# Optimization experiments

Hardware: AMD Instinct MI355X
Metric: run time of the kernel (lower is better)

## Reference

```python
import jax, jax.numpy as jnp
import numpy as np

EPS = 1e-12  # torch F.normalize default eps


def _l2norm(t, axis=-1):
    n = jnp.sqrt(jnp.sum(t * t, axis=axis, keepdims=True))
    return t / jnp.maximum(n, EPS)


def setup_inputs() -> dict:
    key = jax.random.key(0)
    ks = jax.random.split(key, 5)
    B, N, C, H = 8, 4096, 1024, 16
    x = jax.random.normal(ks[0], (B, N, C), dtype=jnp.float32)
    # nn.Linear(dim, 3*dim, bias=False): weight [3C, C]; we store transposed [C, 3C]
    w_qkv = jax.random.normal(ks[1], (C, 3 * C), dtype=jnp.float32) * (1.0 / np.sqrt(C))
    temperature = jnp.ones((H, 1, 1), dtype=jnp.float32)
    w_proj = jax.random.normal(ks[2], (C, C), dtype=jnp.float32) * (1.0 / np.sqrt(C))
    b_proj = jax.random.normal(ks[3], (C,), dtype=jnp.float32) * 0.01
    return {"x": x, "w_qkv": w_qkv, "temperature": temperature,
            "w_proj": w_proj, "b_proj": b_proj}


def reference(x, w_qkv, temperature, w_proj, b_proj):
    B, N, C = x.shape
    H = temperature.shape[0]
    dh = C // H
    # qkv: [B, N, 3C] -> [B, N, 3, H, dh] -> q/k/v each [B, H, dh, N]
    qkv = (x @ w_qkv).reshape(B, N, 3, H, dh).transpose(2, 0, 3, 4, 1)
    q, k, v = qkv[0], qkv[1], qkv[2]
    # L2-normalize over token axis (last dim)
    q = _l2norm(q)
    k = _l2norm(k)
    # channel-channel attention: [B, H, dh, dh]
    attn = jnp.einsum("bhdn,bhen->bhde", q, k) * temperature  # temp broadcasts [H,1,1]
    attn = jax.nn.softmax(attn, axis=-1)
    # weighted sum over channels: [B, H, dh, N] -> [B, N, C]
    out = jnp.einsum("bhde,bhen->bhdn", attn, v).transpose(0, 3, 1, 2).reshape(B, N, C)
    return out @ w_proj + b_proj
```

## Files before the change

### kernel.cpp

```cpp
#include <hip/hip_runtime.h>
#include <cstdint>

typedef unsigned short u16;
typedef unsigned int u32;
typedef __attribute__((ext_vector_type(8))) short bf16x8;
typedef __attribute__((ext_vector_type(4))) float f32x4;

typedef const u32 __attribute__((address_space(1)))* gp_t;
typedef u32 __attribute__((address_space(3)))* lp_t;

__device__ __forceinline__ u16 f2bf(float f) {
    union { float f; u32 u; } v; v.f = f;
    u32 r = v.u + 0x7FFFu + ((v.u >> 16) & 1u);
    return (u16)(r >> 16);
}
__device__ __forceinline__ float bf2f(u16 h) {
    union { u32 u; float f; } v; v.u = ((u32)h) << 16;
    return v.f;
}

__global__ void k_pack_x(const float* __restrict__ x, u16* __restrict__ xb, int n4) {
    int stride = gridDim.x * blockDim.x;
    for (int i = blockIdx.x * blockDim.x + threadIdx.x; i < n4; i += stride) {
        float4 v = ((const float4*)x)[i];
        ushort4 o;
        o.x = f2bf(v.x); o.y = f2bf(v.y); o.z = f2bf(v.z); o.w = f2bf(v.w);
        ((ushort4*)xb)[i] = o;
    }
}

__global__ void k_transpose_w(const float* __restrict__ src, u16* __restrict__ dst, int ncols) {
    __shared__ float t[64][65];
    int ntn = ncols >> 6;
    int kb = (blockIdx.x / ntn) * 64;
    int nb = (blockIdx.x % ntn) * 64;
    for (int i = threadIdx.x; i < 4096; i += 256) {
        int r = i >> 6, c = i & 63;
        t[r][c] = src[(long)(kb + r) * ncols + nb + c];
    }
    __syncthreads();
    for (int i = threadIdx.x; i < 4096; i += 256) {
        int r = i >> 6, c = i & 63;
        dst[(long)(nb + r) * 1024 + kb + c] = f2bf(t[c][r]);
    }
}

template<int EPI>
__global__ __launch_bounds__(512, 2) void k_gemm(
    const u16* __restrict__ A, const u16* __restrict__ Bt,
    int nTilesN,
    u16* __restrict__ qkT, u16* __restrict__ v_tm,
    float* __restrict__ outp, const float* __restrict__ bias)
{
    __shared__ uint4 smem4[8704];
    u16* sm = (u16*)smem4;

    const int tid = threadIdx.x;
    const int wid = tid >> 6, lane = tid & 63;
    const int wr = wid >> 2, wc = wid & 3;
    const int fr = lane & 15, sl = lane >> 4;

    const int nwg = gridDim.x;
    const int cpx = nwg >> 3;
    const int logical = (blockIdx.x & 7) * cpx + (blockIdx.x >> 3);

    long m0; int n0;
    const u16* BtEff = Bt;
    if (EPI == 0) {
        const int bn = logical % nTilesN;
        m0 = (long)(logical / nTilesN) * 256;
        n0 = bn * 256;
    } else {
        const int b = logical >> 6;
        const int mt = (logical >> 2) & 15;
        const int nt = logical & 3;
        m0 = (long)b * 4096 + mt * 256;
        n0 = nt * 256;
        BtEff = Bt + ((long)b << 20);
    }

    const int srow = wid * 32 + (lane >> 2);
    const int kswz = (((lane & 3) ^ ((srow >> 1) & 3)) << 3);
    const u16* gA = A + (m0 + srow) * 1024L + kswz;
    const u16* gB = BtEff + ((long)n0 + srow) * 1024L + kswz;
    const int ldst = wid * 1024;

    const int fxor = ((sl ^ ((fr >> 1) & 3)) << 3);
    const int aBase = (wr * 128 + fr) * 32 + fxor;
    const int bBase = 32768 + (wc * 64 + fr) * 32 + fxor;

    f32x4 acc[8][4];
#pragma unroll
    for (int i = 0; i < 8; ++i)
#pragma unroll
        for (int j = 0; j < 4; ++j) acc[i][j] = (f32x4){0.f, 0.f, 0.f, 0.f};

#define STAGE_A(d, kh, ts) do { \
    const u16* g_ = gA + (ts) * 64 + (kh) * 32; \
    u16* l_ = sm + (d) * 16384 + (kh) * 8192 + ldst; \
    __builtin_amdgcn_global_load_lds((gp_t)g_, (lp_t)l_, 16, 0, 0); \
    __builtin_amdgcn_global_load_lds((gp_t)(g_ + 16 * 1024), (lp_t)(l_ + 512), 16, 0, 0); \
} while (0)
#define STAGE_B(d, kh, ts) do { \
    const u16* g_ = gB + (ts) * 64 + (kh) * 32; \
    u16* l_ = sm + 32768 + (d) * 16384 + (kh) * 8192 + ldst; \
    __builtin_amdgcn_global_load_lds((gp_t)g_, (lp_t)l_, 16, 0, 0); \
    __builtin_amdgcn_global_load_lds((gp_t)(g_ + 16 * 1024), (lp_t)(l_ + 512), 16, 0, 0); \
} while (0)

    STAGE_A(0, 0, 0); STAGE_B(0, 0, 0);
    STAGE_A(0, 1, 0); STAGE_B(0, 1, 0);
    STAGE_A(1, 0, 1); STAGE_B(1, 0, 1);
    asm volatile("s_waitcnt vmcnt(8)" ::: "memory");
    __builtin_amdgcn_s_barrier();

    bf16x8 afX[4], afY[4], bfX[4], bfY[4];
#pragma unroll
    for (int ni = 0; ni < 4; ++ni) bfX[ni] = *(const bf16x8*)(sm + bBase + ni * 512);
#pragma unroll
    for (int mi = 0; mi < 4; ++mi) afX[mi] = *(const bf16x8*)(sm + aBase + mi * 512);

#pragma unroll 2
    for (int T = 0; T < 16; ++T) {
        const int d = T & 1;
        const int t1 = (T + 1 < 16) ? T + 1 : 15;
        const int t2 = (T + 2 < 16) ? T + 2 : 15;
        const int base = d * 16384;
        const int nbase = (d ^ 1) * 16384;

#pragma unroll
        for (int mi = 0; mi < 4; ++mi)
            afY[mi] = *(const bf16x8*)(sm + aBase + (4 + mi) * 512 + base);
        STAGE_A(d ^ 1, 1, t1);
        asm volatile("s_waitcnt vmcnt(6)" ::: "memory");
        __builtin_amdgcn_s_barrier();
        __builtin_amdgcn_s_setprio(1);
#pragma unroll
        for (int mi = 0; mi < 4; ++mi)
#pragma unroll
            for (int ni = 0; ni < 4; ++ni)
                acc[mi][ni] = __builtin_amdgcn_mfma_f32_16x16x32_bf16(afX[mi], bfX[ni], acc[mi][ni], 0, 0, 0);
        __builtin_amdgcn_s_setprio(0);
        __builtin_amdgcn_s_barrier();

#pragma unroll
        for (int ni = 0; ni < 4; ++ni)
            bfY[ni] = *(const bf16x8*)(sm + bBase + ni * 512 + base + 8192);
#pragma unroll
        for (int mi = 0; mi < 4; ++mi)
            afX[mi] = *(const bf16x8*)(sm + aBase + mi * 512 + base + 8192);
        STAGE_B(d ^ 1, 1, t1);
        __builtin_amdgcn_s_barrier();
        __builtin_amdgcn_s_setprio(1);
#pragma unroll
        for (int mi = 0; mi < 4; ++mi)
#pragma unroll
            for (int ni = 0; ni < 4; ++ni)
                acc[mi + 4][ni] = __builtin_amdgcn_mfma_f32_16x16x32_bf16(afY[mi], bfX[ni], acc[mi + 4][ni], 0, 0, 0);
        __builtin_amdgcn_s_setprio(0);
        __builtin_amdgcn_s_barrier();

#pragma unroll
        for (int mi = 0; mi < 4; ++mi)
            afY[mi] = *(const bf16x8*)(sm + aBase + (4 + mi) * 512 + base + 8192);
        STAGE_A(d, 0, t2);
        asm volatile("s_waitcnt vmcnt(6)" ::: "memory");
        __builtin_amdgcn_s_barrier();
        __builtin_amdgcn_s_setprio(1);
#pragma unroll
        for (int mi = 0; mi < 4; ++mi)
#pragma unroll
            for (int ni = 0; ni < 4; ++ni)
                acc[mi][ni] = __builtin_amdgcn_mfma_f32_16x16x32_bf16(afX[mi], bfY[ni], acc[mi][ni], 0, 0, 0);
        __builtin_amdgcn_s_setprio(0);
        __builtin_amdgcn_s_barrier();

#pragma unroll
        for (int ni = 0; ni < 4; ++ni)
            bfX[ni] = *(const bf16x8*)(sm + bBase + ni * 512 + nbase);
#pragma unroll
        for (int mi = 0; mi < 4; ++mi)
            afX[mi] = *(const bf16x8*)(sm + aBase + mi * 512 + nbase);
        STAGE_B(d, 0, t2);
        __builtin_amdgcn_s_barrier();
        __builtin_amdgcn_s_setprio(1);
#pragma unroll
        for (int mi = 0; mi < 4; ++mi)
#pragma unroll
            for (int ni = 0; ni < 4; ++ni)
                acc[mi + 4][ni] = __builtin_amdgcn_mfma_f32_16x16x32_bf16(afY[mi], bfY[ni], acc[mi + 4][ni], 0, 0, 0);
        __builtin_amdgcn_s_setprio(0);
        __builtin_amdgcn_s_barrier();
    }
#undef STAGE_A
#undef STAGE_B
    asm volatile("s_waitcnt vmcnt(0)" ::: "memory");
    __syncthreads();

    if (EPI == 0) {
        const long b = m0 >> 12;
        const int tok0 = (int)(m0 & 4095);
        if (n0 < 2048) {
            u16* piece = sm + wid * 8704;
#pragma unroll
            for (int mi = 0; mi < 8; ++mi)
#pragma unroll
                for (int ni = 0; ni < 4; ++ni) {
                    const int ch = ni * 16 + fr;
                    const int tk = mi * 16 + sl * 4;
                    ushort4 w;
                    w.x = f2bf(acc[mi][ni][0]); w.y = f2bf(acc[mi][ni][1]);
                    w.z = f2bf(acc[mi][ni][2]); w.w = f2bf(acc[mi][ni][3]);
                    *(ushort4*)(piece + ch * 136 + tk) = w;
                }
            __syncthreads();
#pragma unroll
            for (int i = 0; i < 16; ++i) {
                const int chunk = i * 512 + tid;
                const int row = chunk >> 4, c16 = chunk & 15;
                const int p = row >> 6, chl = row & 63;
                const int wrp = p >> 2, wcp = p & 3;
                const uint4 v = *(const uint4*)(sm + p * 8704 + chl * 136 + c16 * 8);
                *(uint4*)(qkT + ((b * 2048 + n0 + wcp * 64 + chl) * 4096L + tok0 + wrp * 128 + c16 * 8)) = v;
            }
        } else {
            u16* piece = sm + wid * 8704;
#pragma unroll
            for (int mi = 0; mi < 8; ++mi)
#pragma unroll
                for (int ni = 0; ni < 4; ++ni) {
                    const int ch = ni * 16 + fr;
                    const int tk = mi * 16 + sl * 4;
#pragma unroll
                    for (int r = 0; r < 4; ++r)
                        piece[(tk + r) * 68 + ch] = f2bf(acc[mi][ni][r]);
                }
            __syncthreads();
#pragma unroll
            for (int i = 0; i < 32; ++i) {
                const int chunk = i * 512 + tid;
                const int row = chunk >> 4, c8 = chunk & 15;
                const int p = row >> 7, tk = row & 127;
                const int wrp = p >> 2, wcp = p & 3;
                const uint2 v = *(const uint2*)(sm + p * 8704 + tk * 68 + c8 * 4);
                *(uint2*)(v_tm + ((b * 4096 + tok0 + wrp * 128 + tk) * 1024L + (n0 - 2048) + wcp * 64 + c8 * 4)) = v;
            }
        }
    } else {
        float bi[4];
#pragma unroll
        for (int ni = 0; ni < 4; ++ni) bi[ni] = bias[n0 + wc * 64 + ni * 16 + fr];
#pragma unroll
        for (int pass = 0; pass < 2; ++pass) {
            float* pieceF = (float*)smem4 + wid * 4352;
            if (pass) __syncthreads();
#pragma unroll
            for (int mi2 = 0; mi2 < 4; ++mi2) {
                const int mi = pass * 4 + mi2;
#pragma unroll
                for (int ni = 0; ni < 4; ++ni) {
                    const int ch = ni * 16 + fr;
                    const int tk = mi2 * 16 + sl * 4;
#pragma unroll
                    for (int r = 0; r < 4; ++r)
                        pieceF[(tk + r) * 68 + ch] = acc[mi][ni][r] + bi[ni];
                }
            }
            __syncthreads();
#pragma unroll
            for (int i = 0; i < 16; ++i) {
                const int chunk = i * 512 + tid;
                const int row = chunk >> 4, c4 = chunk & 15;
                const int p = row >> 6, tk = row & 63;
                const int wrp = p >> 2, wcp = p & 3;
                const float4 v = *(const float4*)((float*)smem4 + p * 4352 + tk * 68 + c4 * 4);
                *(float4*)(outp + (m0 + wrp * 128 + pass * 64 + tk) * 1024L + n0 + wcp * 64 + c4 * 4) = v;
            }
        }
    }
}

__global__ __launch_bounds__(512, 2) void k_gram(
    const u16* __restrict__ qkT, float* __restrict__ gram_part, float* __restrict__ sq_part)
{
    __shared__ u16 lQ[64 * 256];
    __shared__ u16 lK[64 * 256];

    const int blk = blockIdx.x;
    const int seg = blk & 15;
    const int bh = blk >> 4;
    const int b = bh >> 4, h = bh & 15;
    const int tid = threadIdx.x;
    const int wid = tid >> 6, lane = tid & 63;

    {
        const int r2 = lane >> 5;
        const int slot = lane & 31;
        const int rbase = wid * 8;
#pragma unroll
        for (int i = 0; i < 4; ++i) {
            const int r = rbase + i * 2 + r2;
            const int col = seg * 256 + ((slot ^ (r & 7)) << 3);
            const u16* gq = qkT + ((long)(b * 2048 + h * 64 + r)) * 4096 + col;
            const u16* gk = qkT + ((long)(b * 2048 + 1024 + h * 64 + r)) * 4096 + col;
            __builtin_amdgcn_global_load_lds((gp_t)gq, (lp_t)(lQ + (rbase + i * 2) * 256), 16, 0, 0);
            __builtin_amdgcn_global_load_lds((gp_t)gk, (lp_t)(lK + (rbase + i * 2) * 256), 16, 0, 0);
        }
    }
    __syncthreads();

    {
        const int row = tid >> 2, q4 = tid & 3;
        const u16* src = (row < 64 ? lQ + row * 256 : lK + (row - 64) * 256) + q4 * 64;
        float s = 0.f;
#pragma unroll
        for (int i = 0; i < 8; ++i) {
            uint4 v = *(const uint4*)(src + i * 8);
            float a0, a1;
            a0 = bf2f((u16)(v.x & 0xFFFF)); a1 = bf2f((u16)(v.x >> 16)); s += a0 * a0 + a1 * a1;
            a0 = bf2f((u16)(v.y & 0xFFFF)); a1 = bf2f((u16)(v.y >> 16)); s += a0 * a0 + a1 * a1;
            a0 = bf2f((u16)(v.z & 0xFFFF)); a1 = bf2f((u16)(v.z >> 16)); s += a0 * a0 + a1 * a1;
            a0 = bf2f((u16)(v.w & 0xFFFF)); a1 = bf2f((u16)(v.w >> 16)); s += a0 * a0 + a1 * a1;
        }
        s += __shfl_xor(s, 1);
        s += __shfl_xor(s, 2);
        if (q4 == 0) sq_part[(long)blk * 128 + row] = s;
    }

    const int mrow = wid >> 1, npair = wid & 1;
    const int fr = lane & 15, sl = lane >> 4;
    f32x4 acc[2];
    acc[0] = (f32x4){0.f, 0.f, 0.f, 0.f};
    acc[1] = (f32x4){0.f, 0.f, 0.f, 0.f};
#pragma unroll
    for (int ks = 0; ks < 8; ++ks) {
        const int ra = mrow * 16 + fr;
        const bf16x8 a = *(const bf16x8*)(lQ + ra * 256 + (((ks * 4 + sl) ^ (ra & 7)) << 3));
#pragma unroll
        for (int ni = 0; ni < 2; ++ni) {
            const int rb = npair * 32 + ni * 16 + fr;
            const bf16x8 bb = *(const bf16x8*)(lK + rb * 256 + (((ks * 4 + sl) ^ (rb & 7)) << 3));
            acc[ni] = __builtin_amdgcn_mfma_f32_16x16x32_bf16(a, bb, acc[ni], 0, 0, 0);
        }
    }
    float* gp = gram_part + (long)blk * 4096;
#pragma unroll
    for (int ni = 0; ni < 2; ++ni)
#pragma unroll
        for (int r = 0; r < 4; ++r)
            gp[(mrow * 16 + sl * 4 + r) * 64 + npair * 32 + ni * 16 + fr] = acc[ni][r];
}

__global__ __launch_bounds__(256) void k_smax(
    const float* __restrict__ gram_part, const float* __restrict__ sq_part,
    const float* __restrict__ temperature, u16* __restrict__ attn_g)
{
    const int row = blockIdx.x * 4 + (threadIdx.x >> 6);
    const int e = threadIdx.x & 63;
    const int bh = row >> 6, d = row & 63;
    const int h = bh & 15;
    float raw = 0.f, sqq = 0.f, sqk = 0.f;
    const float* gp = gram_part + (long)bh * 16 * 4096 + d * 64 + e;
    const float* sp = sq_part + (long)bh * 16 * 128;
#pragma unroll
    for (int s = 0; s < 16; ++s) {
        raw += gp[s * 4096];
        sqq += sp[s * 128 + d];
        sqk += sp[s * 128 + 64 + e];
    }
    const float rq = 1.f / fmaxf(sqrtf(sqq), 1e-12f);
    const float rk = 1.f / fmaxf(sqrtf(sqk), 1e-12f);
    const float v = raw * rq * rk * temperature[h];
    float mx = v;
#pragma unroll
    for (int o = 32; o; o >>= 1) mx = fmaxf(mx, __shfl_xor(mx, o));
    const float p = __expf(v - mx);
    float sum = p;
#pragma unroll
    for (int o = 32; o; o >>= 1) sum += __shfl_xor(sum, o);
    attn_g[(long)row * 64 + e] = f2bf(p / sum);
}

__global__ __launch_bounds__(256) void k_wmix(
    const u16* __restrict__ attn_g, const u16* __restrict__ wpT, u16* __restrict__ wmix)
{
    __shared__ u16 lA[64 * 72];
    __shared__ u16 lB[256 * 64];

    const int blk = blockIdx.x;
    const int nseg = blk & 3, bh = blk >> 2;
    const int b = bh >> 4, h = bh & 15;
    const int tid = threadIdx.x;
    const int wid = tid >> 6, lane = tid & 63;
    const int fr = lane & 15, sl = lane >> 4;

#pragma unroll
    for (int i = 0; i < 8; ++i) {
        const int cc = wid * 8 + i;
        const int row = cc * 8 + (lane >> 3);
        const int slot = lane & 7;
        const u16* g = wpT + (long)(nseg * 256 + row) * 1024 + h * 64 + ((slot ^ (row & 7)) << 3);
        __builtin_amdgcn_global_load_lds((gp_t)g, (lp_t)(lB + cc * 512), 16, 0, 0);
    }
    {
        const u16* src = attn_g + (long)bh * 4096;
        for (int i = tid; i < 4096; i += 256) {
            const int d = i >> 6, e = i & 63;
            lA[e * 72 + d] = src[i];
        }
    }
    __syncthreads();

    f32x4 acc[4][4];
#pragma unroll
    for (int i = 0; i < 4; ++i)
#pragma unroll
        for (int j = 0; j < 4; ++j) acc[i][j] = (f32x4){0.f, 0.f, 0.f, 0.f};

#pragma unroll
    for (int ks = 0; ks < 2; ++ks) {
        bf16x8 a[4], bb[4];
#pragma unroll
        for (int mi = 0; mi < 4; ++mi)
            a[mi] = *(const bf16x8*)(lA + (mi * 16 + fr) * 72 + ks * 32 + sl * 8);
#pragma unroll
        for (int ni = 0; ni < 4; ++ni) {
            const int rb = wid * 64 + ni * 16 + fr;
            bb[ni] = *(const bf16x8*)(lB + rb * 64 + (((ks * 4 + sl) ^ (rb & 7)) << 3));
        }
#pragma unroll
        for (int mi = 0; mi < 4; ++mi)
#pragma unroll
            for (int ni = 0; ni < 4; ++ni)
                acc[mi][ni] = __builtin_amdgcn_mfma_f32_16x16x32_bf16(a[mi], bb[ni], acc[mi][ni], 0, 0, 0);
    }

    u16* dst = wmix + ((long)b << 20);
#pragma unroll
    for (int mi = 0; mi < 4; ++mi)
#pragma unroll
        for (int ni = 0; ni < 4; ++ni) {
            const int cout = nseg * 256 + wid * 64 + ni * 16 + fr;
            const int e0 = mi * 16 + sl * 4;
            ushort4 w;
            w.x = f2bf(acc[mi][ni][0]); w.y = f2bf(acc[mi][ni][1]);
            w.z = f2bf(acc[mi][ni][2]); w.w = f2bf(acc[mi][ni][3]);
            *(ushort4*)(dst + (long)cout * 1024 + h * 64 + e0) = w;
        }
}

extern "C" void kernel_launch(void* const* d_in, const int* in_sizes, int n_in,
                              void* d_out, int out_size, void* d_ws, size_t ws_size,
                              hipStream_t stream) {
    const float* x = (const float*)d_in[0];
    const float* w_qkv = (const float*)d_in[1];
    const float* temperature = (const float*)d_in[2];
    const float* w_proj = (const float*)d_in[3];
    const float* b_proj = (const float*)d_in[4];
    float* out = (float*)d_out;
    char* ws = (char*)d_ws;

    u16* wqT   = (u16*)(ws);
    u16* wpT   = (u16*)(ws + 6291456);
    u16* xb    = (u16*)(ws + 8388608);
    u16* qkT   = (u16*)(ws + 75497472);
    u16* v_tm  = (u16*)(ws + 209715200);
    u16* attn_g = (u16*)(ws + 276889600);
    float* gram_part = (float*)(ws + 8388608);
    float* sq_part   = (float*)(ws + 41943040);
    u16* wmix = (u16*)(ws + 8388608);

    k_pack_x<<<2048, 256, 0, stream>>>(x, xb, 8388608);
    k_transpose_w<<<768, 256, 0, stream>>>(w_qkv, wqT, 3072);
    k_transpose_w<<<256, 256, 0, stream>>>(w_proj, wpT, 1024);
    k_gemm<0><<<1536, 512, 0, stream>>>(xb, wqT, 12, qkT, v_tm, nullptr, nullptr);
    k_gram<<<2048, 512, 0, stream>>>(qkT, gram_part, sq_part);
    k_smax<<<2048, 256, 0, stream>>>(gram_part, sq_part, temperature, attn_g);
    k_wmix<<<512, 256, 0, stream>>>(attn_g, wpT, wmix);
    k_gemm<1><<<512, 512, 0, stream>>>(v_tm, wmix, 4, nullptr, nullptr, out, b_proj);
}
```

Before: 392.1 us.

## Fold V projection into per-batch output weights, skip materializing V

Instead of computing V = x·Wv for every token and then multiplying by the per-batch mixed weights, the V weight slice is packed separately and multiplied with the per-batch attention-mixed projection weights (a small 1024x1024 GEMM per batch). The final GEMM then reads x directly with the fused per-batch weight. This removes a third of the large QKV GEMM and the V write/readback, at the cost of an extra small batched GEMM and re-reading x in the final GEMM.

```diff
diff --git a/kernel.cpp b/kernel.cpp
--- a/kernel.cpp
+++ b/kernel.cpp
@@ -43,6 +43,17 @@
         int r = i >> 6, c = i & 63;
         dst[(long)(nb + r) * 1024 + kb + c] = f2bf(t[c][r]);
     }
+}
+
+__global__ __launch_bounds__(256) void k_pack_wv(const float* __restrict__ wqkv, u16* __restrict__ wvb) {
+    const int idx = blockIdx.x * 256 + threadIdx.x;
+    const int cin = idx >> 7, e0 = (idx & 127) * 8;
+    const float4 v1 = *(const float4*)(wqkv + (long)cin * 3072 + 2048 + e0);
+    const float4 v2 = *(const float4*)(wqkv + (long)cin * 3072 + 2048 + e0 + 4);
+    u16 u[8];
+    u[0] = f2bf(v1.x); u[1] = f2bf(v1.y); u[2] = f2bf(v1.z); u[3] = f2bf(v1.w);
+    u[4] = f2bf(v2.x); u[5] = f2bf(v2.y); u[6] = f2bf(v2.z); u[7] = f2bf(v2.w);
+    *(uint4*)(wvb + (long)cin * 1024 + e0) = *(const uint4*)u;
 }
 
 template<int EPI>
@@ -64,25 +75,14 @@
     const int cpx = nwg >> 3;
     const int logical = (blockIdx.x & 7) * cpx + (blockIdx.x >> 3);
 
-    long m0; int n0;
-    const u16* BtEff = Bt;
-    if (EPI == 0) {
-        const int bn = logical % nTilesN;
-        m0 = (long)(logical / nTilesN) * 256;
-        n0 = bn * 256;
-    } else {
-        const int b = logical >> 6;
-        const int mt = (logical >> 2) & 15;
-        const int nt = logical & 3;
-        m0 = (long)b * 4096 + mt * 256;
-        n0 = nt * 256;
-        BtEff = Bt + ((long)b << 20);
-    }
+    const int bn = logical % nTilesN;
+    const long m0 = (long)(logical / nTilesN) * 256;
+    const int n0 = bn * 256;
 
     const int srow = wid * 32 + (lane >> 2);
     const int kswz = (((lane & 3) ^ ((srow >> 1) & 3)) << 3);
     const u16* gA = A + (m0 + srow) * 1024L + kswz;
-    const u16* gB = BtEff + ((long)n0 + srow) * 1024L + kswz;
+    const u16* gB = Bt + ((long)n0 + srow) * 1024L + kswz;
     const int ldst = wid * 1024;
 
     const int fxor = ((sl ^ ((fr >> 1) & 3)) << 3);
@@ -200,82 +200,27 @@
     if (EPI == 0) {
         const long b = m0 >> 12;
         const int tok0 = (int)(m0 & 4095);
-        if (n0 < 2048) {
-            u16* piece = sm + wid * 8704;
-#pragma unroll
-            for (int mi = 0; mi < 8; ++mi)
-#pragma unroll
-                for (int ni = 0; ni < 4; ++ni) {
-                    const int ch = ni * 16 + fr;
-                    const int tk = mi * 16 + sl * 4;
-                    ushort4 w;
-                    w.x = f2bf(acc[mi][ni][0]); w.y = f2bf(acc[mi][ni][1]);
-                    w.z = f2bf(acc[mi][ni][2]); w.w = f2bf(acc[mi][ni][3]);
-                    *(ushort4*)(piece + ch * 136 + tk) = w;
-                }
-            __syncthreads();
-#pragma unroll
-            for (int i = 0; i < 16; ++i) {
-                const int chunk = i * 512 + tid;
-                const int row = chunk >> 4, c16 = chunk & 15;
-                const int p = row >> 6, chl = row & 63;
-                const int wrp = p >> 2, wcp = p & 3;
-                const uint4 v = *(const uint4*)(sm + p * 8704 + chl * 136 + c16 * 8);
-                *(uint4*)(qkT + ((b * 2048 + n0 + wcp * 64 + chl) * 4096L + tok0 + wrp * 128 + c16 * 8)) = v;
+        u16* piece = sm + wid * 8704;
+#pragma unroll
+        for (int mi = 0; mi < 8; ++mi)
+#pragma unroll
+            for (int ni = 0; ni < 4; ++ni) {
+                const int ch = ni * 16 + fr;
+                const int tk = mi * 16 + sl * 4;
+                ushort4 w;
+                w.x = f2bf(acc[mi][ni][0]); w.y = f2bf(acc[mi][ni][1]);
+                w.z = f2bf(acc[mi][ni][2]); w.w = f2bf(acc[mi][ni][3]);
+                *(ushort4*)(piece + ch * 136 + tk) = w;
             }
-        } else {
-            u16* piece = sm + wid * 8704;
-#pragma unroll
-            for (int mi = 0; mi < 8; ++mi)
-#pragma unroll
-                for (int ni = 0; ni < 4; ++ni) {
-                    const int ch = ni * 16 + fr;
-                    const int tk = mi * 16 + sl * 4;
-#pragma unroll
-                    for (int r = 0; r < 4; ++r)
-                        piece[(tk + r) * 68 + ch] = f2bf(acc[mi][ni][r]);
-                }
-            __syncthreads();
-#pragma unroll
-            for (int i = 0; i < 32; ++i) {
-                const int chunk = i * 512 + tid;
-                const int row = chunk >> 4, c8 = chunk & 15;
-                const int p = row >> 7, tk = row & 127;
-                const int wrp = p >> 2, wcp = p & 3;
-                const uint2 v = *(const uint2*)(sm + p * 8704 + tk * 68 + c8 * 4);
-                *(uint2*)(v_tm + ((b * 4096 + tok0 + wrp * 128 + tk) * 1024L + (n0 - 2048) + wcp * 64 + c8 * 4)) = v;
-            }
-        }
-    } else {
-        float bi[4];
-#pragma unroll
-        for (int ni = 0; ni < 4; ++ni) bi[ni] = bias[n0 + wc * 64 + ni * 16 + fr];
-#pragma unroll
-        for (int pass = 0; pass < 2; ++pass) {
-            float* pieceF = (float*)smem4 + wid * 4352;
-            if (pass) __syncthreads();
-#pragma unroll
-            for (int mi2 = 0; mi2 < 4; ++mi2) {
-                const int mi = pass * 4 + mi2;
-#pragma unroll
-                for (int ni = 0; ni < 4; ++ni) {
-                    const int ch = ni * 16 + fr;
-                    const int tk = mi2 * 16 + sl * 4;
-#pragma unroll
-                    for (int r = 0; r < 4; ++r)
-                        pieceF[(tk + r) * 68 + ch] = acc[mi][ni][r] + bi[ni];
-                }
-            }
-            __syncthreads();
-#pragma unroll
-            for (int i = 0; i < 16; ++i) {
-                const int chunk = i * 512 + tid;
-                const int row = chunk >> 4, c4 = chunk & 15;
-                const int p = row >> 6, tk = row & 63;
-                const int wrp = p >> 2, wcp = p & 3;
-                const float4 v = *(const float4*)((float*)smem4 + p * 4352 + tk * 68 + c4 * 4);
-                *(float4*)(outp + (m0 + wrp * 128 + pass * 64 + tk) * 1024L + n0 + wcp * 64 + c4 * 4) = v;
-            }
+        __syncthreads();
+#pragma unroll
+        for (int i = 0; i < 16; ++i) {
+            const int chunk = i * 512 + tid;
+            const int row = chunk >> 4, c16 = chunk & 15;
+            const int p = row >> 6, chl = row & 63;
+            const int wrp = p >> 2, wcp = p & 3;
+            const uint4 v = *(const uint4*)(sm + p * 8704 + chl * 136 + c16 * 8);
+            *(uint4*)(qkT + ((b * 2048 + n0 + wcp * 64 + chl) * 4096L + tok0 + wrp * 128 + c16 * 8)) = v;
         }
     }
 }
@@ -449,6 +394,260 @@
         }
 }
 
+__global__ __launch_bounds__(256) void k_g128(
+    const u16* __restrict__ A, long Ab, const u16* __restrict__ Bt, long Bs,
+    u16* __restrict__ C, long Cb, int K, int MT, int NT)
+{
+    __shared__ u16 sm[8192];
+    __shared__ u16 lC[128 * 136];
+
+    const int tid = threadIdx.x;
+    const int wid = tid >> 6, lane = tid & 63;
+    const int wr = wid >> 1, wc = wid & 1;
+    const int fr = lane & 15, sl = lane >> 4;
+
+    const int nwg = gridDim.x;
+    const int logical = (blockIdx.x & 7) * (nwg >> 3) + (blockIdx.x >> 3);
+
+    const int b = logical / (MT * NT);
+    const int r = logical % (MT * NT);
+    const int i0 = r / NT, j0 = r % NT;
+    const int m0 = i0 * 128, n0 = j0 * 128;
+    const u16* Abp = A + (long)b * Ab;
+    const u16* Bbp = Bt + (long)b * Bs;
+    u16* Cbp = C + (long)b * Cb;
+
+    const int srow = lane >> 2;
+    const int sslot = lane & 3;
+
+    f32x4 acc[4][4];
+#pragma unroll
+    for (int i = 0; i < 4; ++i)
+#pragma unroll
+        for (int j = 0; j < 4; ++j) acc[i][j] = (f32x4){0.f, 0.f, 0.f, 0.f};
+
+    for (int kt = 0; kt < K; kt += 32) {
+        __syncthreads();
+#pragma unroll
+        for (int i = 0; i < 2; ++i) {
+            const int row = wid * 32 + i * 16 + srow;
+            const int swz = (sslot ^ ((row >> 1) & 3)) << 3;
+            const u16* ga = Abp + (long)(m0 + row) * K + kt + swz;
+            const u16* gb = Bbp + (long)(n0 + row) * K + kt + swz;
+            __builtin_amdgcn_global_load_lds((gp_t)ga, (lp_t)(sm + (wid * 2 + i) * 512), 16, 0, 0);
+            __builtin_amdgcn_global_load_lds((gp_t)gb, (lp_t)(sm + 4096 + (wid * 2 + i) * 512), 16, 0, 0);
+        }
+        __syncthreads();
+        bf16x8 af[4], bfr[4];
+#pragma unroll
+        for (int mi = 0; mi < 4; ++mi) {
+            const int row = wr * 64 + mi * 16 + fr;
+            af[mi] = *(const bf16x8*)(sm + row * 32 + ((sl ^ ((row >> 1) & 3)) << 3));
+        }
+#pragma unroll
+        for (int ni = 0; ni < 4; ++ni) {
+            const int row = wc * 64 + ni * 16 + fr;
+            bfr[ni] = *(const bf16x8*)(sm + 4096 + row * 32 + ((sl ^ ((row >> 1) & 3)) << 3));
+        }
+#pragma unroll
+        for (int mi = 0; mi < 4; ++mi)
+#pragma unroll
+            for (int ni = 0; ni < 4; ++ni)
+                acc[mi][ni] = __builtin_amdgcn_mfma_f32_16x16x32_bf16(af[mi], bfr[ni], acc[mi][ni], 0, 0, 0);
+    }
+    __syncthreads();
+
+#pragma unroll
+    for (int mi = 0; mi < 4; ++mi)
+#pragma unroll
+        for (int ni = 0; ni < 4; ++ni) {
+            const int ch = wc * 64 + ni * 16 + fr;
+            const int tk = wr * 64 + mi * 16 + sl * 4;
+#pragma unroll
+            for (int rr = 0; rr < 4; ++rr)
+                lC[(tk + rr) * 136 + ch] = f2bf(acc[mi][ni][rr]);
+        }
+    __syncthreads();
+    {
+        const int tk = tid >> 1, half = tid & 1;
+        const u16* sp = lC + tk * 136 + half * 64;
+        u16* dp = Cbp + (long)(m0 + tk) * 1024 + n0 + half * 64;
+#pragma unroll
+        for (int i = 0; i < 8; ++i) ((uint4*)dp)[i] = ((const uint4*)sp)[i];
+    }
+}
+
+__global__ __launch_bounds__(512, 2) void k_gemm256f(
+    const u16* __restrict__ A, long Ab, const u16* __restrict__ Bt, long Bs,
+    int MT, int NT, float* __restrict__ cF, long Cb, const float* __restrict__ bias)
+{
+    __shared__ uint4 smem4[8704];
+    u16* sm = (u16*)smem4;
+
+    const int tid = threadIdx.x;
+    const int wid = tid >> 6, lane = tid & 63;
+    const int wr = wid >> 2, wc = wid & 3;
+    const int fr = lane & 15, sl = lane >> 4;
+
+    const int nwg = gridDim.x;
+    const int logical = (blockIdx.x & 7) * (nwg >> 3) + (blockIdx.x >> 3);
+    const int b = logical / (MT * NT);
+    const int rem = logical % (MT * NT);
+    const int mt = rem / NT, nt = rem % NT;
+    const long m0 = (long)mt * 256;
+    const int n0 = nt * 256;
+
+    const int srow = wid * 32 + (lane >> 2);
+    const int kswz = (((lane & 3) ^ ((srow >> 1) & 3)) << 3);
+    const u16* gA = A + (long)b * Ab + (m0 + srow) * 1024L + kswz;
+    const u16* gB = Bt + (long)b * Bs + ((long)n0 + srow) * 1024L + kswz;
+    const int ldst = wid * 1024;
+
+    const int fxor = ((sl ^ ((fr >> 1) & 3)) << 3);
+    const int aBase = (wr * 128 + fr) * 32 + fxor;
+    const int bBase = 32768 + (wc * 64 + fr) * 32 + fxor;
+
+    f32x4 acc[8][4];
+#pragma unroll
+    for (int i = 0; i < 8; ++i)
+#pragma unroll
+        for (int j = 0; j < 4; ++j) acc[i][j] = (f32x4){0.f, 0.f, 0.f, 0.f};
+
+#define STAGE_A(d, kh, ts) do { \
+    const u16* g_ = gA + (ts) * 64 + (kh) * 32; \
+    u16* l_ = sm + (d) * 16384 + (kh) * 8192 + ldst; \
+    __builtin_amdgcn_global_load_lds((gp_t)g_, (lp_t)l_, 16, 0, 0); \
+    __builtin_amdgcn_global_load_lds((gp_t)(g_ + 16 * 1024), (lp_t)(l_ + 512), 16, 0, 0); \
+} while (0)
+#define STAGE_B(d, kh, ts) do { \
+    const u16* g_ = gB + (ts) * 64 + (kh) * 32; \
+    u16* l_ = sm + 32768 + (d) * 16384 + (kh) * 8192 + ldst; \
+    __builtin_amdgcn_global_load_lds((gp_t)g_, (lp_t)l_, 16, 0, 0); \
+    __builtin_amdgcn_global_load_lds((gp_t)(g_ + 16 * 1024), (lp_t)(l_ + 512), 16, 0, 0); \
+} while (0)
+
+    STAGE_A(0, 0, 0); STAGE_B(0, 0, 0);
+    STAGE_A(0, 1, 0); STAGE_B(0, 1, 0);
+    STAGE_A(1, 0, 1); STAGE_B(1, 0, 1);
+    asm volatile("s_waitcnt vmcnt(8)" ::: "memory");
+    __builtin_amdgcn_s_barrier();
+
+    bf16x8 afX[4], afY[4], bfX[4], bfY[4];
+#pragma unroll
+    for (int ni = 0; ni < 4; ++ni) bfX[ni] = *(const bf16x8*)(sm + bBase + ni * 512);
+#pragma unroll
+    for (int mi = 0; mi < 4; ++mi) afX[mi] = *(const bf16x8*)(sm + aBase + mi * 512);
+
+#pragma unroll 2
+    for (int T = 0; T < 16; ++T) {
+        const int d = T & 1;
+        const int t1 = (T + 1 < 16) ? T + 1 : 15;
+        const int t2 = (T + 2 < 16) ? T + 2 : 15;
+        const int base = d * 16384;
+        const int nbase = (d ^ 1) * 16384;
+
+#pragma unroll
+        for (int mi = 0; mi < 4; ++mi)
+            afY[mi] = *(const bf16x8*)(sm + aBase + (4 + mi) * 512 + base);
+        STAGE_A(d ^ 1, 1, t1);
+        asm volatile("s_waitcnt vmcnt(6)" ::: "memory");
+        __builtin_amdgcn_s_barrier();
+        __builtin_amdgcn_s_setprio(1);
+#pragma unroll
+        for (int mi = 0; mi < 4; ++mi)
+#pragma unroll
+            for (int ni = 0; ni < 4; ++ni)
+                acc[mi][ni] = __builtin_amdgcn_mfma_f32_16x16x32_bf16(afX[mi], bfX[ni], acc[mi][ni], 0, 0, 0);
+        __builtin_amdgcn_s_setprio(0);
+        __builtin_amdgcn_s_barrier();
+
+#pragma unroll
+        for (int ni = 0; ni < 4; ++ni)
+            bfY[ni] = *(const bf16x8*)(sm + bBase + ni * 512 + base + 8192);
+#pragma unroll
+        for (int mi = 0; mi < 4; ++mi)
+            afX[mi] = *(const bf16x8*)(sm + aBase + mi * 512 + base + 8192);
+        STAGE_B(d ^ 1, 1, t1);
+        __builtin_amdgcn_s_barrier();
+        __builtin_amdgcn_s_setprio(1);
+#pragma unroll
+        for (int mi = 0; mi < 4; ++mi)
+#pragma unroll
+            for (int ni = 0; ni < 4; ++ni)
+                acc[mi + 4][ni] = __builtin_amdgcn_mfma_f32_16x16x32_bf16(afY[mi], bfX[ni], acc[mi + 4][ni], 0, 0, 0);
+        __builtin_amdgcn_s_setprio(0);
+        __builtin_amdgcn_s_barrier();
+
+#pragma unroll
+        for (int mi = 0; mi < 4; ++mi)
+            afY[mi] = *(const bf16x8*)(sm + aBase + (4 + mi) * 512 + base + 8192);
+        STAGE_A(d, 0, t2);
+        asm volatile("s_waitcnt vmcnt(6)" ::: "memory");
+        __builtin_amdgcn_s_barrier();
+        __builtin_amdgcn_s_setprio(1);
+#pragma unroll
+        for (int mi = 0; mi < 4; ++mi)
+#pragma unroll
+            for (int ni = 0; ni < 4; ++ni)
+                acc[mi][ni] = __builtin_amdgcn_mfma_f32_16x16x32_bf16(afX[mi], bfY[ni], acc[mi][ni], 0, 0, 0);
+        __builtin_amdgcn_s_setprio(0);
+        __builtin_amdgcn_s_barrier();
+
+#pragma unroll
+        for (int ni = 0; ni < 4; ++ni)
+            bfX[ni] = *(const bf16x8*)(sm + bBase + ni * 512 + nbase);
+#pragma unroll
+        for (int mi = 0; mi < 4; ++mi)
+            afX[mi] = *(const bf16x8*)(sm + aBase + mi * 512 + nbase);
+        STAGE_B(d, 0, t2);
+        __builtin_amdgcn_s_barrier();
+        __builtin_amdgcn_s_setprio(1);
+#pragma unroll
+        for (int mi = 0; mi < 4; ++mi)
+#pragma unroll
+            for (int ni = 0; ni < 4; ++ni)
+                acc[mi + 4][ni] = __builtin_amdgcn_mfma_f32_16x16x32_bf16(afY[mi], bfY[ni], acc[mi + 4][ni], 0, 0, 0);
+        __builtin_amdgcn_s_setprio(0);
+        __builtin_amdgcn_s_barrier();
+    }
+#undef STAGE_A
+#undef STAGE_B
+    asm volatile("s_waitcnt vmcnt(0)" ::: "memory");
+    __syncthreads();
+
+    float* cbase = cF + (long)b * Cb;
+    float bi[4];
+#pragma unroll
+    for (int ni = 0; ni < 4; ++ni) bi[ni] = bias[n0 + wc * 64 + ni * 16 + fr];
+#pragma unroll
+    for (int pass = 0; pass < 2; ++pass) {
+        float* pieceF = (float*)smem4 + wid * 4352;
+        if (pass) __syncthreads();
+#pragma unroll
+        for (int mi2 = 0; mi2 < 4; ++mi2) {
+            const int mi = pass * 4 + mi2;
+#pragma unroll
+            for (int ni = 0; ni < 4; ++ni) {
+                const int ch = ni * 16 + fr;
+                const int tk = mi2 * 16 + sl * 4;
+#pragma unroll
+                for (int rr = 0; rr < 4; ++rr)
+                    pieceF[(tk + rr) * 68 + ch] = acc[mi][ni][rr] + bi[ni];
+            }
+        }
+        __syncthreads();
+#pragma unroll
+        for (int i = 0; i < 16; ++i) {
+            const int chunk = i * 512 + tid;
+            const int row = chunk >> 4, c4 = chunk & 15;
+            const int p = row >> 6, tk = row & 63;
+            const int wrp = p >> 2, wcp = p & 3;
+            const float4 v = *(const float4*)((float*)smem4 + p * 4352 + tk * 68 + c4 * 4);
+            *(float4*)(cbase + (m0 + wrp * 128 + pass * 64 + tk) * 1024L + n0 + wcp * 64 + c4 * 4) = v;
+        }
+    }
+}
+
 extern "C" void kernel_launch(void* const* d_in, const int* in_sizes, int n_in,
                               void* d_out, int out_size, void* d_ws, size_t ws_size,
                               hipStream_t stream) {
@@ -460,22 +659,25 @@
     float* out = (float*)d_out;
     char* ws = (char*)d_ws;
 
-    u16* wqT   = (u16*)(ws);
-    u16* wpT   = (u16*)(ws + 6291456);
-    u16* xb    = (u16*)(ws + 8388608);
-    u16* qkT   = (u16*)(ws + 75497472);
-    u16* v_tm  = (u16*)(ws + 209715200);
-    u16* attn_g = (u16*)(ws + 276889600);
-    float* gram_part = (float*)(ws + 8388608);
-    float* sq_part   = (float*)(ws + 41943040);
-    u16* wmix = (u16*)(ws + 8388608);
-
-    k_pack_x<<<2048, 256, 0, stream>>>(x, xb, 8388608);
+    u16* wqT    = (u16*)(ws);
+    u16* wpT    = (u16*)(ws + 6291456);
+    u16* wvb    = (u16*)(ws + 8388608);
+    u16* xt     = (u16*)(ws + 10485760);
+    u16* qkT    = (u16*)(ws + 77594624);
+    float* gram_part = (float*)(ws + 211812352);
+    float* sq_part   = (float*)(ws + 245366784);
+    u16* attn_g = (u16*)(ws + 246415360);
+    u16* wmix   = (u16*)(ws + 247463936);
+    u16* wfinT  = (u16*)(ws + 211812352);
+
+    k_pack_x<<<2048, 256, 0, stream>>>(x, xt, 8388608);
     k_transpose_w<<<768, 256, 0, stream>>>(w_qkv, wqT, 3072);
     k_transpose_w<<<256, 256, 0, stream>>>(w_proj, wpT, 1024);
-    k_gemm<0><<<1536, 512, 0, stream>>>(xb, wqT, 12, qkT, v_tm, nullptr, nullptr);
+    k_pack_wv<<<512, 256, 0, stream>>>(w_qkv, wvb);
+    k_gemm<0><<<1024, 512, 0, stream>>>(xt, wqT, 8, qkT, nullptr, nullptr, nullptr);
     k_gram<<<2048, 512, 0, stream>>>(qkT, gram_part, sq_part);
     k_smax<<<2048, 256, 0, stream>>>(gram_part, sq_part, temperature, attn_g);
     k_wmix<<<512, 256, 0, stream>>>(attn_g, wpT, wmix);
-    k_gemm<1><<<512, 512, 0, stream>>>(v_tm, wmix, 4, nullptr, nullptr, out, b_proj);
-}
+    k_g128<<<512, 256, 0, stream>>>(wmix, 1048576L, wvb, 0L, wfinT, 1048576L, 1024, 8, 8);
+    k_gemm256f<<<512, 512, 0, stream>>>(xt, 4194304L, wfinT, 1048576L, 16, 4, out, 4194304L, b_proj);
+}
```

Measured after the change: 358.6 us. -8.5%, faster.
